# Optimization experiments

Measured on AMD Instinct MI355X. Metric: run time of the kernel, lower is better.

Reference implementation:

```python
import jax, jax.numpy as jnp
import numpy as np

B, H, N, T = 16, 16, 4096, 8
D_S, D_ID, L, K = 256, 128, 8, 32
HS, DQ = 8, 32
D_HID = 1024
D_STEER = 3 * D_S + D_ID  # cat(s_cur, id_cur, walker_state, token_embed)


def _gelu(x):
    return jax.nn.gelu(x, approximate=False)


def _rms(x, w):
    return x * jax.lax.rsqrt(jnp.mean(x * x, axis=-1, keepdims=True) + 1e-6) * w


def _mlp2(x, w1, b1, w2, b2):
    return _gelu(x @ w1 + b1) @ w2 + b2


def _per_plane_mlp(x, plane_idx, W1, b1, W2, b2):
    # x: [n, D_in]; plane_idx: [n] int in [0,L). Vectorized plane dispatch:
    # compute all planes then select (avoids data-dependent masking).
    h_all = jnp.einsum('nd,phd->nph', x, W1) + b1[None]          # [n,L,D_hid]
    h = jnp.take_along_axis(h_all, plane_idx[:, None, None], axis=1)[:, 0]
    h = _gelu(h)
    o_all = jnp.einsum('nh,pdh->npd', h, W2) + b2[None]          # [n,L,D_out]
    return jnp.take_along_axis(o_all, plane_idx[:, None, None], axis=1)[:, 0]


def setup_inputs() -> dict:
    key = jax.random.key(0)
    ks = jax.random.split(key, 16)
    f = jax.random.normal
    return {
        's': f(ks[0], (B, N, D_S), jnp.float32),
        'node_id': f(ks[1], (N, D_ID), jnp.float32),
        'walker_state': f(ks[2], (B, H, D_S), jnp.float32),
        'token_embed': f(ks[3], (B, T, D_S), jnp.float32),
        'norm_w': jnp.ones((D_S,), jnp.float32),
        'W1': f(ks[4], (L, D_HID, D_STEER), jnp.float32) * 0.014,
        'b1': jnp.zeros((L, D_HID), jnp.float32),
        'W2': f(ks[5], (L, D_S, D_HID), jnp.float32) * (2.0 / D_HID) ** 0.5,
        'b2': jnp.zeros((L, D_S), jnp.float32),
        'qw1': f(ks[6], (D_STEER, 2 * HS * DQ), jnp.float32) * 0.014,
        'qb1': jnp.zeros((2 * HS * DQ,), jnp.float32),
        'qw2': f(ks[7], (2 * HS * DQ, HS * DQ), jnp.float32) * 0.02,
        'qb2': jnp.zeros((HS * DQ,), jnp.float32),
        'kw1': f(ks[8], (D_ID, 2 * HS * DQ), jnp.float32) * 0.014,
        'kb1': jnp.zeros((2 * HS * DQ,), jnp.float32),
        'kw2': f(ks[9], (2 * HS * DQ, HS * DQ), jnp.float32) * 0.02,
        'kb2': jnp.zeros((HS * DQ,), jnp.float32),
        'walker_pos': jax.random.randint(ks[10], (B, H), 0, N, jnp.int32),
        'plane_idx': jax.random.randint(ks[11], (B, H), 0, L, jnp.int32),
        'neighbors': jax.random.randint(ks[12], (N, K), 0, N, jnp.int32),
    }


def reference(s, node_id, walker_state, token_embed, norm_w, W1, b1, W2, b2,
              qw1, qb1, qw2, qb2, kw1, kb1, kw2, kb2,
              walker_pos, plane_idx, neighbors):
    b_idx = jnp.arange(B)[:, None]            # [B,1] batch gather index
    plane_flat = plane_idx.reshape(-1)        # [B*H], constant per walker
    scale = 1.0 / (HS * np.sqrt(DQ).astype(np.float32))

    def step(carry, tok):
        s, pos, wstate, co, vc, lb = carry
        s_cur = s[b_idx, pos]                 # gather [B,H,D_s]
        id_cur = node_id[pos]                 # [B,H,D_id]
        s_n = _rms(s_cur, norm_w)
        tok_b = jnp.broadcast_to(tok[:, None, :], (B, H, D_S))
        steer = jnp.concatenate([s_n, id_cur, wstate, tok_b], axis=-1)  # [B,H,D_steer]
        # per-plane content MLP (dispatch by plane index)
        content = _per_plane_mlp(steer.reshape(B * H, D_STEER), plane_flat,
                                 W1, b1, W2, b2).reshape(B, H, D_S)
        # shared q/k projections and neighbor scoring
        q = _mlp2(steer, qw1, qb1, qw2, qb2).reshape(B, H, HS, DQ)
        nbr = neighbors[pos]                  # [B,H,K]
        k = _mlp2(node_id[nbr], kw1, kb1, kw2, kb2).reshape(B, H, K, HS, DQ)
        scores = jnp.einsum('bhsd,bhksd->bhk', q, k) * scale   # [B,H,K]
        probs = jax.nn.softmax(scores, axis=-1)
        mp = probs.mean(axis=(0, 1))
        lb = lb + K * jnp.sum(mp * mp)        # load-balance penalty
        # non-differentiable hop: argmax move
        sel = jnp.argmax(scores, axis=-1)     # [B,H]
        next_pos = jnp.take_along_axis(nbr, sel[..., None], axis=-1)[..., 0]
        # state updates: scatter content into s, residual walker state
        s_new = s.at[b_idx, pos].add(content)
        wstate_new = wstate + content
        # non-grad co-visit / visit-count accumulators
        pf = pos.reshape(-1)
        nf = next_pos.reshape(-1)
        co = co.at[pf, nf].add(1.0)
        vc = vc.at[nf].add(1.0)
        motor = wstate_new.mean(axis=1)       # [B,D_s]
        return (s_new, next_pos, wstate_new, co, vc, lb), motor

    init = (s, walker_pos, walker_state,
            jnp.zeros((N, N), jnp.float32), jnp.zeros((N,), jnp.float32),
            jnp.float32(0.0))
    (s_new, pos_new, ws_new, co, vc, lb), motors = jax.lax.scan(
        step, init, token_embed.transpose(1, 0, 2))
    motor_bt = motors.transpose(1, 0, 2)      # [B,T,D_s]
    return motor_bt, s_new, pos_new, ws_new, co, vc, lb
```

## Files before the change

kernel.cpp:

```cpp
#include <hip/hip_runtime.h>
#include <math.h>

#define B_    16
#define H_    16
#define N_    4096
#define T_    8
#define DS_   256
#define DID_  128
#define L_    8
#define K_    32
#define DHID_ 1024
#define DSTEER_ 896
#define QH_   512
#define QO_   256
#define NW_   256
#define SLOTS_ 512
#define SCORE_SCALE 0.022097086912079608f

struct KArgs {
    const float *s_in, *node_id, *ws_in, *token, *norm_w;
    const float *W1, *b1, *W2, *b2;
    const float *qw1, *qb1, *qw2, *qb2, *kw1, *kb1, *kw2, *kb2;
    const int *walker_pos, *plane_idx, *neighbors;
    float *out_motor, *out_s, *out_pos, *out_ws, *out_co, *out_vc, *out_lb;
    float *keys, *kh, *steer, *steerT, *h1p, *q1p, *c2p, *q2p, *mp_all;
    int *pos, *plane_order, *chunk_plane, *chunk_rows, *slot_of, *nchunks;
};

__device__ __forceinline__ float gelu_exact(float x) {
    return 0.5f * x * (1.0f + erff(x * 0.70710678118654752f));
}

#define FMA4(c, b, a) { c.x = fmaf(b.x, (a), c.x); c.y = fmaf(b.y, (a), c.y); \
                        c.z = fmaf(b.z, (a), c.z); c.w = fmaf(b.w, (a), c.w); }

__device__ __forceinline__ void gelu4(float4& v) {
    v.x = gelu_exact(v.x); v.y = gelu_exact(v.y);
    v.z = gelu_exact(v.z); v.w = gelu_exact(v.w);
}

__device__ __forceinline__ void rgemm_inner(
    const float* __restrict__ a0, const float* __restrict__ a1,
    const float* bp, int ldb, int K,
    float4& c0, float4& c1)
{
    for (int k = 0; k < K; k += 8) {
        const float4 a0l = *reinterpret_cast<const float4*>(a0 + k);
        const float4 a0h = *reinterpret_cast<const float4*>(a0 + k + 4);
        const float4 a1l = *reinterpret_cast<const float4*>(a1 + k);
        const float4 a1h = *reinterpret_cast<const float4*>(a1 + k + 4);
        const float* b8 = bp + (size_t)k * ldb;
#define KSTEP(o, av0, av1) { float4 bv = *reinterpret_cast<const float4*>(b8 + (size_t)(o) * ldb); \
                             FMA4(c0, bv, av0); FMA4(c1, bv, av1); }
        KSTEP(0, a0l.x, a1l.x)
        KSTEP(1, a0l.y, a1l.y)
        KSTEP(2, a0l.z, a1l.z)
        KSTEP(3, a0l.w, a1l.w)
        KSTEP(4, a0h.x, a1h.x)
        KSTEP(5, a0h.y, a1h.y)
        KSTEP(6, a0h.z, a1h.z)
        KSTEP(7, a0h.w, a1h.w)
#undef KSTEP
    }
}


__global__ __launch_bounds__(256) void setup1_kernel(KArgs a)
{
    int bid = blockIdx.x, tid = threadIdx.x;
    if (bid < 4096) {
        int gid = bid * 256 + tid, stride = 4096 * 256;
        const float4 z = {0.f, 0.f, 0.f, 0.f};
        float4* co4 = reinterpret_cast<float4*>(a.out_co);
        float4* s4o = reinterpret_cast<float4*>(a.out_s);
        const float4* s4i = reinterpret_cast<const float4*>(a.s_in);
        for (int i = gid; i < 4194304; i += stride) co4[i] = z;
        for (int i = gid; i < 4194304; i += stride) s4o[i] = s4i[i];
        float4* m4 = reinterpret_cast<float4*>(a.out_motor);
        for (int i = gid; i < 8192; i += stride) m4[i] = z;
        float4* w4o = reinterpret_cast<float4*>(a.out_ws);
        const float4* w4i = reinterpret_cast<const float4*>(a.ws_in);
        for (int i = gid; i < 16384; i += stride) w4o[i] = w4i[i];
        float4* v4 = reinterpret_cast<float4*>(a.out_vc);
        for (int i = gid; i < 1024; i += stride) v4[i] = z;
        if (gid == 0) a.out_lb[0] = 0.f;
    } else if (bid == 4096) {
        a.pos[tid] = a.walker_pos[tid];
        a.mp_all[tid] = 0.f;
        __shared__ int cnt_s[8];
        __shared__ int cplane_s[16], cbase_s[16];
        __shared__ int nch_s;
        int wave = tid >> 6, lane = tid & 63;
        for (int pp = wave; pp < 8; pp += 4) {
            int base = 0;
            for (int c0 = 0; c0 < NW_; c0 += 64) {
                int w = c0 + lane;
                bool hit = (a.plane_idx[w] == pp);
                unsigned long long mask = __ballot(hit);
                if (hit) {
                    int rank = __popcll(mask & ((1ull << lane) - 1ull));
                    a.plane_order[pp * NW_ + base + rank] = w;
                }
                base += __popcll(mask);
            }
            if (lane == 0) cnt_s[pp] = base;
        }
        __syncthreads();
        if (tid == 0) {
            int nc = 0;
            for (int p = 0; p < 8; ++p)
                for (int s0 = 0; s0 < cnt_s[p]; s0 += 32) {
                    cplane_s[nc] = p; cbase_s[nc] = s0; ++nc;
                }
            *a.nchunks = nc;
            nch_s = nc;
        }
        __syncthreads();
        int nc = nch_s;
        for (int idx = tid; idx < 512; idx += 256) {
            int c = idx >> 5, i = idx & 31;
            int v = -1;
            if (c < nc) {
                int p = cplane_s[c];
                int r = cbase_s[c] + i;
                if (r < cnt_s[p]) v = a.plane_order[p * NW_ + r];
            }
            a.chunk_rows[c * 32 + i] = v;
            if (v >= 0) a.slot_of[v] = c * 32 + i;
            if (i == 0) a.chunk_plane[c] = (c < nc) ? cplane_s[c] : 0;
        }
    } else {
        int u = bid - 4097;
        int rt = u >> 3, ct = u & 7;
        int tr = tid >> 4, tc = tid & 15;
        int row = rt * 32 + tr * 2, col = ct * 64 + tc * 4;
        const float* a0 = a.node_id + (size_t)row * DID_;
        float4 c0 = {0.f,0.f,0.f,0.f}, c1 = {0.f,0.f,0.f,0.f};
        rgemm_inner(a0, a0 + DID_, a.kw1 + col, QH_, DID_, c0, c1);
        float4 bv = *reinterpret_cast<const float4*>(a.kb1 + col);
        c0.x += bv.x; c0.y += bv.y; c0.z += bv.z; c0.w += bv.w;
        c1.x += bv.x; c1.y += bv.y; c1.z += bv.z; c1.w += bv.w;
        gelu4(c0); gelu4(c1);
        *reinterpret_cast<float4*>(a.kh + (size_t)row * QH_ + col) = c0;
        *reinterpret_cast<float4*>(a.kh + (size_t)(row + 1) * QH_ + col) = c1;
    }
}


__device__ void dev_steer(const KArgs& a, int w, int tid, int t) {
    int b = w >> 4;
    int p = a.pos[w];
    int slot = a.slot_of[w];
    float sc = a.out_s[((size_t)b * N_ + p) * DS_ + tid];
    float v = sc * sc;
    for (int off = 32; off > 0; off >>= 1) v += __shfl_down(v, off);
    __shared__ float red[4];
    if ((tid & 63) == 0) red[tid >> 6] = v;
    __syncthreads();
    float tot = red[0] + red[1] + red[2] + red[3];
    float r = rsqrtf(tot * (1.0f / DS_) + 1e-6f);
    float* st = a.steer + (size_t)w * DSTEER_;
    float v0 = sc * r * a.norm_w[tid];
    float v2 = a.out_ws[(size_t)w * DS_ + tid];
    float v3 = a.token[((size_t)b * T_ + t) * DS_ + tid];
    st[tid] = v0;
    st[384 + tid] = v2;
    st[640 + tid] = v3;
    a.steerT[(size_t)tid * SLOTS_ + slot] = v0;
    a.steerT[(size_t)(384 + tid) * SLOTS_ + slot] = v2;
    a.steerT[(size_t)(640 + tid) * SLOTS_ + slot] = v3;
    if (tid < 128) {
        float v1 = a.node_id[(size_t)p * DID_ + tid];
        st[256 + tid] = v1;
        a.steerT[(size_t)(256 + tid) * SLOTS_ + slot] = v1;
    }
}


__global__ __launch_bounds__(256) void setup2_kernel(KArgs a)
{
    int bid = blockIdx.x, tid = threadIdx.x;
    if (bid < 512) {
        int rt = bid >> 2, ct = bid & 3;
        int tr = tid >> 4, tc = tid & 15;
        int row = rt * 32 + tr * 2, col = ct * 64 + tc * 4;
        const float* a0 = a.kh + (size_t)row * QH_;
        float4 c0 = {0.f,0.f,0.f,0.f}, c1 = {0.f,0.f,0.f,0.f};
        rgemm_inner(a0, a0 + QH_, a.kw2 + col, QO_, QH_, c0, c1);
        float4 bv = *reinterpret_cast<const float4*>(a.kb2 + col);
        c0.x += bv.x; c0.y += bv.y; c0.z += bv.z; c0.w += bv.w;
        c1.x += bv.x; c1.y += bv.y; c1.z += bv.z; c1.w += bv.w;
        *reinterpret_cast<float4*>(a.keys + (size_t)row * QO_ + col) = c0;
        *reinterpret_cast<float4*>(a.keys + (size_t)(row + 1) * QO_ + col) = c1;
    } else {
        dev_steer(a, bid - 512, tid, 0);
    }
}

__global__ __launch_bounds__(256) void steer_kernel(KArgs a, int t)
{
    dev_steer(a, blockIdx.x, threadIdx.x, t);
}


__global__ __launch_bounds__(256) void l1_kernel(KArgs a)
{
    __shared__ float bs[112 * 64];
    int bid = blockIdx.x, tid = threadIdx.x;
    float4 c0 = {0.f,0.f,0.f,0.f}, c1 = {0.f,0.f,0.f,0.f};
    if (bid < 512) {
        int kp = bid & 7, tile = bid >> 3;
        int rt = tile >> 3, ct = tile & 7;
        int tr = tid >> 4, tc = tid & 15;
        int row = rt * 32 + tr * 2, col0 = ct * 64;
#pragma unroll
        for (int i = 0; i < 7; ++i) {
            int idx = tid + i * 256;
            int kk = idx >> 4, c4 = (idx & 15) << 2;
            *reinterpret_cast<float4*>(bs + kk * 64 + c4) =
                *reinterpret_cast<const float4*>(a.qw1 + (size_t)(kp * 112 + kk) * QH_ + col0 + c4);
        }
        __syncthreads();
        const float* a0 = a.steer + (size_t)row * DSTEER_ + kp * 112;
        rgemm_inner(a0, a0 + DSTEER_, bs + tc * 4, 64, 112, c0, c1);
        float* o = a.q1p + (size_t)kp * 131072;
        int col = col0 + tc * 4;
        *reinterpret_cast<float4*>(o + (size_t)row * QH_ + col) = c0;
        *reinterpret_cast<float4*>(o + (size_t)(row + 1) * QH_ + col) = c1;
    } else {
        int b2 = bid - 512;
        int kp = b2 & 7, tile = b2 >> 3;
        int c = tile >> 4, jt = tile & 15;
        if (c >= *a.nchunks) return;
        int p = a.chunk_plane[c];
        int tr = tid >> 3, tc = tid & 7;
        int J = jt * 64 + tr * 2;
#pragma unroll
        for (int i = 0; i < 4; ++i) {
            int idx = tid + i * 256;
            if (idx < 896) {
                int kk = idx >> 3, s4 = (idx & 7) << 2;
                *reinterpret_cast<float4*>(bs + kk * 32 + s4) =
                    *reinterpret_cast<const float4*>(a.steerT + (size_t)(kp * 112 + kk) * SLOTS_ + c * 32 + s4);
            }
        }
        __syncthreads();
        const float* a0 = a.W1 + ((size_t)p * DHID_ + J) * DSTEER_ + kp * 112;
        rgemm_inner(a0, a0 + DSTEER_, bs + tc * 4, 32, 112, c0, c1);
        float* o = a.h1p + (size_t)kp * 524288;
        int slot = c * 32 + tc * 4;
        *reinterpret_cast<float4*>(o + (size_t)J * SLOTS_ + slot) = c0;
        *reinterpret_cast<float4*>(o + (size_t)(J + 1) * SLOTS_ + slot) = c1;
    }
}


__global__ __launch_bounds__(256) void l2f_kernel(KArgs a)
{
    __shared__ float smem[4096];
    int bid = blockIdx.x, tid = threadIdx.x;
    float4 c0 = {0.f,0.f,0.f,0.f}, c1 = {0.f,0.f,0.f,0.f};
    if (bid < 256) {
        int kp = bid & 7, tile = bid >> 3;
        int rt = tile >> 2, ct = tile & 3;
        int tr = tid >> 4, tc = tid & 15;
        int row0 = rt * 32, col = ct * 64 + tc * 4;
#pragma unroll
        for (int i = 0; i < 2; ++i) {
            int idx = tid + i * 256;
            int r = idx >> 4, k4 = (idx & 15) << 2;
            size_t off = (size_t)(row0 + r) * QH_ + kp * 64 + k4;
            float4 acc = *reinterpret_cast<const float4*>(a.qb1 + kp * 64 + k4);
#pragma unroll
            for (int p8 = 0; p8 < 8; ++p8) {
                float4 v = *reinterpret_cast<const float4*>(a.q1p + (size_t)p8 * 131072 + off);
                acc.x += v.x; acc.y += v.y; acc.z += v.z; acc.w += v.w;
            }
            gelu4(acc);
            *reinterpret_cast<float4*>(smem + r * 72 + k4) = acc;
        }
        __syncthreads();
        const float* a0 = smem + (tr * 2) * 72;
        rgemm_inner(a0, a0 + 72, a.qw2 + (size_t)(kp * 64) * QO_ + col, QO_, 64, c0, c1);
        float* o = a.q2p + (size_t)kp * 65536;
        int row = row0 + tr * 2;
        *reinterpret_cast<float4*>(o + (size_t)row * QO_ + col) = c0;
        *reinterpret_cast<float4*>(o + (size_t)(row + 1) * QO_ + col) = c1;
    } else {
        int b2i = bid - 256;
        int kp = b2i & 7, tile = b2i >> 3;
        int c = tile >> 2, jt = tile & 3;
        if (c >= *a.nchunks) return;
        int p = a.chunk_plane[c];
        int tr = tid >> 3, tc = tid & 7;
        int J = jt * 64 + tr * 2;
#pragma unroll
        for (int i = 0; i < 4; ++i) {
            int idx = tid + i * 256;
            int kk = idx >> 3, s4 = (idx & 7) << 2;
            int kq = kp * 128 + kk;
            size_t off = (size_t)kq * SLOTS_ + c * 32 + s4;
            float bj = a.b1[p * DHID_ + kq];
            float4 acc = {bj, bj, bj, bj};
#pragma unroll
            for (int p8 = 0; p8 < 8; ++p8) {
                float4 v = *reinterpret_cast<const float4*>(a.h1p + (size_t)p8 * 524288 + off);
                acc.x += v.x; acc.y += v.y; acc.z += v.z; acc.w += v.w;
            }
            gelu4(acc);
            *reinterpret_cast<float4*>(smem + kk * 32 + s4) = acc;
        }
        __syncthreads();
        const float* a0 = a.W2 + ((size_t)p * DS_ + J) * DHID_ + kp * 128;
        rgemm_inner(a0, a0 + DHID_, smem + tc * 4, 32, 128, c0, c1);
        float* o = a.c2p + (size_t)kp * 131072;
        int slot = c * 32 + tc * 4;
        *reinterpret_cast<float4*>(o + (size_t)J * SLOTS_ + slot) = c0;
        *reinterpret_cast<float4*>(o + (size_t)(J + 1) * SLOTS_ + slot) = c1;
    }
}


__global__ __launch_bounds__(256) void score_kernel(KArgs a, int t)
{
    int w = blockIdx.x;
    int b = w >> 4;
    int tid = threadIdx.x;
    int pold = a.pos[w];
    int slot = a.slot_of[w];
    __shared__ float qv_s[256];
    __shared__ int nbr_s[32];
    __shared__ float part_s[8][32];
    __shared__ float sc_s[32];
    if (tid < 32) nbr_s[tid] = a.neighbors[(size_t)pold * K_ + tid];
    float qsum = a.qb2[tid];
#pragma unroll
    for (int kp = 0; kp < 8; ++kp) qsum += a.q2p[(size_t)kp * 65536 + (size_t)w * QO_ + tid];
    qv_s[tid] = qsum;
    float csum = a.b2[a.chunk_plane[slot >> 5] * DS_ + tid];
#pragma unroll
    for (int kp = 0; kp < 8; ++kp) csum += a.c2p[(size_t)kp * 131072 + (size_t)tid * SLOTS_ + slot];
    __syncthreads();
    int k = tid & 31, part = tid >> 5;
    int nk = nbr_s[k];
    const float* kp_ = a.keys + (size_t)nk * 256 + part * 32;
    const float* qp = qv_s + part * 32;
    float acc = 0.f;
#pragma unroll
    for (int i = 0; i < 32; i += 4) {
        float4 kv = *reinterpret_cast<const float4*>(kp_ + i);
        acc += kv.x * qp[i] + kv.y * qp[i+1] + kv.z * qp[i+2] + kv.w * qp[i+3];
    }
    part_s[part][k] = acc;
    __syncthreads();
    if (tid < 32) {
        float s = 0.f;
#pragma unroll
        for (int p8 = 0; p8 < 8; ++p8) s += part_s[p8][tid];
        sc_s[tid] = s * SCORE_SCALE;
    }
    __syncthreads();
    if (tid < 32) {
        float sv = sc_s[tid];
        float m = sv;
        for (int off = 1; off < 32; off <<= 1) m = fmaxf(m, __shfl_xor(m, off));
        float e = expf(sv - m);
        float ssum = e;
        for (int off = 1; off < 32; off <<= 1) ssum += __shfl_xor(ssum, off);
        float prob = e / ssum;
        atomicAdd(&a.mp_all[t * 32 + tid], prob);
        float bs = sv; int bi = tid;
        for (int off = 1; off < 32; off <<= 1) {
            float os = __shfl_xor(bs, off);
            int   oi = __shfl_xor(bi, off);
            if (os > bs || (os == bs && oi < bi)) { bs = os; bi = oi; }
        }
        if (tid == 0) {
            int next = nbr_s[bi];
            a.pos[w] = next;
            if (t == T_ - 1) a.out_pos[w] = (float)next;
            atomicAdd(&a.out_co[(size_t)pold * N_ + next], 1.0f);
            atomicAdd(&a.out_vc[next], 1.0f);
        }
    }
    atomicAdd(&a.out_s[((size_t)b * N_ + pold) * DS_ + tid], csum);
    float wn = a.out_ws[(size_t)w * DS_ + tid] + csum;
    a.out_ws[(size_t)w * DS_ + tid] = wn;
    atomicAdd(&a.out_motor[((size_t)b * T_ + t) * DS_ + tid], wn * (1.0f / H_));
}

__global__ __launch_bounds__(256) void final_kernel(KArgs a)
{
    int tid = threadIdx.x;
    float v = a.mp_all[tid] * (1.0f / 256.f);
    v = v * v;
    for (int off = 32; off > 0; off >>= 1) v += __shfl_down(v, off);
    __shared__ float red[4];
    if ((tid & 63) == 0) red[tid >> 6] = v;
    __syncthreads();
    if (tid == 0) a.out_lb[0] = (float)K_ * (red[0] + red[1] + red[2] + red[3]);
}


extern "C" void kernel_launch(void* const* d_in, const int* in_sizes, int n_in,
                              void* d_out, int out_size, void* d_ws, size_t ws_size,
                              hipStream_t stream)
{
    KArgs a;
    a.s_in    = (const float*)d_in[0];
    a.node_id = (const float*)d_in[1];
    a.ws_in   = (const float*)d_in[2];
    a.token   = (const float*)d_in[3];
    a.norm_w  = (const float*)d_in[4];
    a.W1  = (const float*)d_in[5];
    a.b1  = (const float*)d_in[6];
    a.W2  = (const float*)d_in[7];
    a.b2  = (const float*)d_in[8];
    a.qw1 = (const float*)d_in[9];
    a.qb1 = (const float*)d_in[10];
    a.qw2 = (const float*)d_in[11];
    a.qb2 = (const float*)d_in[12];
    a.kw1 = (const float*)d_in[13];
    a.kb1 = (const float*)d_in[14];
    a.kw2 = (const float*)d_in[15];
    a.kb2 = (const float*)d_in[16];
    a.walker_pos = (const int*)d_in[17];
    a.plane_idx  = (const int*)d_in[18];
    a.neighbors  = (const int*)d_in[19];

    float* out = (float*)d_out;
    a.out_motor = out;
    a.out_s     = a.out_motor + 32768;
    a.out_pos   = a.out_s + (size_t)16777216;
    a.out_ws    = a.out_pos + 256;
    a.out_co    = a.out_ws + 65536;
    a.out_vc    = a.out_co + (size_t)16777216;
    a.out_lb    = a.out_vc + 4096;

    float* ws = (float*)d_ws;
    a.keys   = ws;
    a.steer  = a.keys + 1048576;
    a.steerT = a.steer + 229376;
    a.h1p    = a.steerT + 458752;
    a.kh     = a.h1p;
    a.q1p    = a.h1p + 4194304;
    a.c2p    = a.q1p + 1048576;
    a.q2p    = a.c2p + 1048576;
    a.mp_all = a.q2p + 524288;
    a.pos         = (int*)(a.mp_all + 256);
    a.plane_order = a.pos + 256;
    a.chunk_plane = a.plane_order + 2048;
    a.chunk_rows  = a.chunk_plane + 16;
    a.slot_of     = a.chunk_rows + 512;
    a.nchunks     = a.slot_of + 256;

    setup1_kernel<<<4096 + 1 + 1024, 256, 0, stream>>>(a);
    setup2_kernel<<<512 + 256, 256, 0, stream>>>(a);
    for (int t = 0; t < T_; ++t) {
        l1_kernel<<<2560, 256, 0, stream>>>(a);
        l2f_kernel<<<768, 256, 0, stream>>>(a);
        score_kernel<<<256, 256, 0, stream>>>(a, t);
        if (t < T_ - 1) steer_kernel<<<256, 256, 0, stream>>>(a, t + 1);
    }
    final_kernel<<<1, 256, 0, stream>>>(a);
}
```

Baseline: 548.4 us.

## Use 8x4 register tiles in GEMM kernels and move output init to memset/memcpy

The l1 and l2f GEMM paths now use a per-thread 8-row by 4-column register tile (rgemm_8x4) instead of 2x4, which cuts the grid sizes and raises arithmetic per loaded value. The setup zeroing and copy of co, vc, lb, motor, s and walker state move out of the kernel into hipMemsetAsync and device-to-device hipMemcpyAsync calls. The aim is to reduce per-step launch and block overhead and redundant B-operand reloads, at the cost of fewer blocks, less parallelism and more registers per thread. The single memset over co plus vc plus lb relies on those outputs sitting contiguously in memory.

After: 630.4 us. 1.15x slower.

```diff
diff --git a/kernel.cpp b/kernel.cpp
--- a/kernel.cpp
+++ b/kernel.cpp
@@ -64,27 +64,34 @@
     }
 }
 
+__device__ __forceinline__ void rgemm_8x4(
+    const float* __restrict__ A, size_t lda,
+    const float* Bs, int ldb, int K, float4 acc[8])
+{
+    for (int k = 0; k < K; k += 4) {
+        float4 a[8];
+#pragma unroll
+        for (int r = 0; r < 8; ++r)
+            a[r] = *reinterpret_cast<const float4*>(A + (size_t)r * lda + k);
+        const float* b = Bs + k * ldb;
+#pragma unroll
+        for (int kk = 0; kk < 4; ++kk) {
+            float4 bv = *reinterpret_cast<const float4*>(b + kk * ldb);
+#pragma unroll
+            for (int r = 0; r < 8; ++r) {
+                float av = (kk == 0) ? a[r].x : (kk == 1) ? a[r].y
+                         : (kk == 2) ? a[r].z : a[r].w;
+                FMA4(acc[r], bv, av);
+            }
+        }
+    }
+}
+
 
 __global__ __launch_bounds__(256) void setup1_kernel(KArgs a)
 {
     int bid = blockIdx.x, tid = threadIdx.x;
-    if (bid < 4096) {
-        int gid = bid * 256 + tid, stride = 4096 * 256;
-        const float4 z = {0.f, 0.f, 0.f, 0.f};
-        float4* co4 = reinterpret_cast<float4*>(a.out_co);
-        float4* s4o = reinterpret_cast<float4*>(a.out_s);
-        const float4* s4i = reinterpret_cast<const float4*>(a.s_in);
-        for (int i = gid; i < 4194304; i += stride) co4[i] = z;
-        for (int i = gid; i < 4194304; i += stride) s4o[i] = s4i[i];
-        float4* m4 = reinterpret_cast<float4*>(a.out_motor);
-        for (int i = gid; i < 8192; i += stride) m4[i] = z;
-        float4* w4o = reinterpret_cast<float4*>(a.out_ws);
-        const float4* w4i = reinterpret_cast<const float4*>(a.ws_in);
-        for (int i = gid; i < 16384; i += stride) w4o[i] = w4i[i];
-        float4* v4 = reinterpret_cast<float4*>(a.out_vc);
-        for (int i = gid; i < 1024; i += stride) v4[i] = z;
-        if (gid == 0) a.out_lb[0] = 0.f;
-    } else if (bid == 4096) {
+    if (bid == 0) {
         a.pos[tid] = a.walker_pos[tid];
         a.mp_all[tid] = 0.f;
         __shared__ int cnt_s[8];
@@ -130,7 +137,7 @@
             if (i == 0) a.chunk_plane[c] = (c < nc) ? cplane_s[c] : 0;
         }
     } else {
-        int u = bid - 4097;
+        int u = bid - 1;
         int rt = u >> 3, ct = u & 7;
         int tr = tid >> 4, tc = tid & 15;
         int row = rt * 32 + tr * 2, col = ct * 64 + tc * 4;
@@ -205,36 +212,41 @@
 
 __global__ __launch_bounds__(256) void l1_kernel(KArgs a)
 {
-    __shared__ float bs[112 * 64];
+    __shared__ float bs[112 * 32];
     int bid = blockIdx.x, tid = threadIdx.x;
-    float4 c0 = {0.f,0.f,0.f,0.f}, c1 = {0.f,0.f,0.f,0.f};
-    if (bid < 512) {
-        int kp = bid & 7, tile = bid >> 3;
-        int rt = tile >> 3, ct = tile & 7;
-        int tr = tid >> 4, tc = tid & 15;
-        int row = rt * 32 + tr * 2, col0 = ct * 64;
-#pragma unroll
-        for (int i = 0; i < 7; ++i) {
+    int tr = tid >> 3, tc = tid & 7;
+    float4 acc[8];
+#pragma unroll
+    for (int r = 0; r < 8; ++r) acc[r] = make_float4(0.f, 0.f, 0.f, 0.f);
+
+    if (bid < 128) {
+        int kp = bid & 7, ct = bid >> 3;
+        int col0 = ct * 32;
+#pragma unroll
+        for (int i = 0; i < 4; ++i) {
             int idx = tid + i * 256;
-            int kk = idx >> 4, c4 = (idx & 15) << 2;
-            *reinterpret_cast<float4*>(bs + kk * 64 + c4) =
-                *reinterpret_cast<const float4*>(a.qw1 + (size_t)(kp * 112 + kk) * QH_ + col0 + c4);
-        }
-        __syncthreads();
-        const float* a0 = a.steer + (size_t)row * DSTEER_ + kp * 112;
-        rgemm_inner(a0, a0 + DSTEER_, bs + tc * 4, 64, 112, c0, c1);
+            if (idx < 896) {
+                int kk = idx >> 3, c4 = (idx & 7) << 2;
+                *reinterpret_cast<float4*>(bs + kk * 32 + c4) =
+                    *reinterpret_cast<const float4*>(a.qw1 + (size_t)(kp * 112 + kk) * QH_ + col0 + c4);
+            }
+        }
+        __syncthreads();
+        int w0 = tr * 8;
+        rgemm_8x4(a.steer + (size_t)w0 * DSTEER_ + kp * 112, DSTEER_,
+                  bs + tc * 4, 32, 112, acc);
         float* o = a.q1p + (size_t)kp * 131072;
         int col = col0 + tc * 4;
-        *reinterpret_cast<float4*>(o + (size_t)row * QH_ + col) = c0;
-        *reinterpret_cast<float4*>(o + (size_t)(row + 1) * QH_ + col) = c1;
+#pragma unroll
+        for (int r = 0; r < 8; ++r)
+            *reinterpret_cast<float4*>(o + (size_t)(w0 + r) * QH_ + col) = acc[r];
     } else {
-        int b2 = bid - 512;
+        int b2 = bid - 128;
         int kp = b2 & 7, tile = b2 >> 3;
-        int c = tile >> 4, jt = tile & 15;
+        int c = tile >> 2, jt = tile & 3;
         if (c >= *a.nchunks) return;
         int p = a.chunk_plane[c];
-        int tr = tid >> 3, tc = tid & 7;
-        int J = jt * 64 + tr * 2;
+        int J0 = jt * 256;
 #pragma unroll
         for (int i = 0; i < 4; ++i) {
             int idx = tid + i * 256;
@@ -245,12 +257,14 @@
             }
         }
         __syncthreads();
-        const float* a0 = a.W1 + ((size_t)p * DHID_ + J) * DSTEER_ + kp * 112;
-        rgemm_inner(a0, a0 + DSTEER_, bs + tc * 4, 32, 112, c0, c1);
+        int J = J0 + tr * 8;
+        rgemm_8x4(a.W1 + ((size_t)p * DHID_ + J) * DSTEER_ + kp * 112, DSTEER_,
+                  bs + tc * 4, 32, 112, acc);
         float* o = a.h1p + (size_t)kp * 524288;
         int slot = c * 32 + tc * 4;
-        *reinterpret_cast<float4*>(o + (size_t)J * SLOTS_ + slot) = c0;
-        *reinterpret_cast<float4*>(o + (size_t)(J + 1) * SLOTS_ + slot) = c1;
+#pragma unroll
+        for (int r = 0; r < 8; ++r)
+            *reinterpret_cast<float4*>(o + (size_t)(J + r) * SLOTS_ + slot) = acc[r];
     }
 }
 
@@ -259,12 +273,12 @@
 {
     __shared__ float smem[4096];
     int bid = blockIdx.x, tid = threadIdx.x;
-    float4 c0 = {0.f,0.f,0.f,0.f}, c1 = {0.f,0.f,0.f,0.f};
     if (bid < 256) {
         int kp = bid & 7, tile = bid >> 3;
         int rt = tile >> 2, ct = tile & 3;
         int tr = tid >> 4, tc = tid & 15;
         int row0 = rt * 32, col = ct * 64 + tc * 4;
+        float4 c0 = {0.f,0.f,0.f,0.f}, c1 = {0.f,0.f,0.f,0.f};
 #pragma unroll
         for (int i = 0; i < 2; ++i) {
             int idx = tid + i * 256;
@@ -288,12 +302,13 @@
         *reinterpret_cast<float4*>(o + (size_t)(row + 1) * QO_ + col) = c1;
     } else {
         int b2i = bid - 256;
-        int kp = b2i & 7, tile = b2i >> 3;
-        int c = tile >> 2, jt = tile & 3;
+        int kp = b2i & 7, c = b2i >> 3;
         if (c >= *a.nchunks) return;
         int p = a.chunk_plane[c];
         int tr = tid >> 3, tc = tid & 7;
-        int J = jt * 64 + tr * 2;
+        float4 acc8[8];
+#pragma unroll
+        for (int r = 0; r < 8; ++r) acc8[r] = make_float4(0.f, 0.f, 0.f, 0.f);
 #pragma unroll
         for (int i = 0; i < 4; ++i) {
             int idx = tid + i * 256;
@@ -311,12 +326,14 @@
             *reinterpret_cast<float4*>(smem + kk * 32 + s4) = acc;
         }
         __syncthreads();
-        const float* a0 = a.W2 + ((size_t)p * DS_ + J) * DHID_ + kp * 128;
-        rgemm_inner(a0, a0 + DHID_, smem + tc * 4, 32, 128, c0, c1);
+        int J = tr * 8;
+        rgemm_8x4(a.W2 + ((size_t)p * DS_ + J) * DHID_ + kp * 128, DHID_,
+                  smem + tc * 4, 32, 128, acc8);
         float* o = a.c2p + (size_t)kp * 131072;
         int slot = c * 32 + tc * 4;
-        *reinterpret_cast<float4*>(o + (size_t)J * SLOTS_ + slot) = c0;
-        *reinterpret_cast<float4*>(o + (size_t)(J + 1) * SLOTS_ + slot) = c1;
+#pragma unroll
+        for (int r = 0; r < 8; ++r)
+            *reinterpret_cast<float4*>(o + (size_t)(J + r) * SLOTS_ + slot) = acc8[r];
     }
 }
 
@@ -454,11 +471,18 @@
     a.slot_of     = a.chunk_rows + 512;
     a.nchunks     = a.slot_of + 256;
 
-    setup1_kernel<<<4096 + 1 + 1024, 256, 0, stream>>>(a);
+    hipMemsetAsync(a.out_motor, 0, 32768 * sizeof(float), stream);
+    hipMemsetAsync(a.out_co, 0, (size_t)(16777216 + 4096 + 1) * sizeof(float), stream);
+    hipMemcpyAsync(a.out_s, a.s_in, (size_t)16777216 * sizeof(float),
+                   hipMemcpyDeviceToDevice, stream);
+    hipMemcpyAsync(a.out_ws, a.ws_in, (size_t)65536 * sizeof(float),
+                   hipMemcpyDeviceToDevice, stream);
+
+    setup1_kernel<<<1 + 1024, 256, 0, stream>>>(a);
     setup2_kernel<<<512 + 256, 256, 0, stream>>>(a);
     for (int t = 0; t < T_; ++t) {
-        l1_kernel<<<2560, 256, 0, stream>>>(a);
-        l2f_kernel<<<768, 256, 0, stream>>>(a);
+        l1_kernel<<<128 + 512, 256, 0, stream>>>(a);
+        l2f_kernel<<<256 + 128, 256, 0, stream>>>(a);
         score_kernel<<<256, 256, 0, stream>>>(a, t);
         if (t < T_ - 1) steer_kernel<<<256, 256, 0, stream>>>(a, t + 1);
     }
```
